# Optimization experiments

Measured on AMD Instinct MI355X. Metric: run time of the kernel, lower is better.

Reference implementation:

```python
import jax, jax.numpy as jnp
import numpy as np

B, S, H0G, H1G, H0E, H1E, A, E = 16384, 512, 512, 256, 1024, 512, 64, 4


def setup_inputs() -> dict:
    key = jax.random.key(0)
    ks = jax.random.split(key, 8)
    rn = lambda k, shape, s=0.05: jax.random.normal(k, shape, jnp.float32) * s
    return {
        "x": rn(ks[0], (B, S), 1.0),
        # Gating network params (Normalizer + 2 tanh layers + fca, softmax outside)
        "g_mean": jnp.zeros((S,), jnp.float32),
        "g_std": jnp.ones((S,), jnp.float32),
        "gW0": rn(ks[1], (S, H0G)), "gb0": jnp.zeros((H0G,), jnp.float32),
        "gW1": rn(ks[2], (H0G, H1G)), "gb1": jnp.zeros((H1G,), jnp.float32),
        "gWa": rn(ks[3], (H1G, E)), "gba": jnp.zeros((E,), jnp.float32),
        # 4 expert Actors, weights stacked along leading expert axis E
        "e_mean": jnp.zeros((E, S), jnp.float32),
        "e_std": jnp.ones((E, S), jnp.float32),
        "eW0": rn(ks[4], (E, S, H0E)), "eb0": jnp.zeros((E, H0E), jnp.float32),
        "eW1": rn(ks[5], (E, H0E, H1E)), "eb1": jnp.zeros((E, H1E), jnp.float32),
        "eWa": rn(ks[6], (E, H1E, A), 0.001), "eba": jnp.zeros((E, A), jnp.float32),
        "scale": jnp.ones((A,), jnp.float32),  # (a_max - a_min) / 2
    }


def reference(x, g_mean, g_std, gW0, gb0, gW1, gb1, gWa, gba,
              e_mean, e_std, eW0, eb0, eW1, eb1, eWa, eba, scale):
    # Gating: normalize -> tanh MLP -> linear -> softmax over experts
    xg = (x - g_mean) / g_std                                   # [B,S]
    h = jnp.tanh(xg @ gW0 + gb0)
    h = jnp.tanh(h @ gW1 + gb1)
    w = jax.nn.softmax(h @ gWa + gba, axis=-1)                  # [B,E]

    # Experts (Actor.forward), batched over expert axis e
    xe = (x[None, :, :] - e_mean[:, None, :]) / e_std[:, None, :]          # [E,B,S]
    he = jnp.tanh(jnp.einsum('ebs,esh->ebh', xe, eW0) + eb0[:, None, :])   # [E,B,H0E]
    he = jnp.tanh(jnp.einsum('ebh,ehk->ebk', he, eW1) + eb1[:, None, :])   # [E,B,H1E]
    a = (jnp.einsum('ebk,eka->eba', he, eWa) + eba[:, None, :]) * scale    # [E,B,A]

    # Weighted combination of expert action means
    return jnp.einsum('be,eba->ba', w, a)                       # [B,A]
```

## Files before the change

kernel.cpp:

```cpp
#include <hip/hip_runtime.h>
#include <hip/hip_bf16.h>

typedef _Float16 f16;
typedef _Float16 f16x4 __attribute__((ext_vector_type(4)));
typedef _Float16 f16x8 __attribute__((ext_vector_type(8)));
typedef float f32x4 __attribute__((ext_vector_type(4)));

#define DEV static __device__ __forceinline__

DEV void gld_lds16(const void* g, void* l) {
  __builtin_amdgcn_global_load_lds(
      (const __attribute__((address_space(1))) void*)g,
      (__attribute__((address_space(3))) void*)l, 16, 0, 0);
}

DEV float fast_tanh(float x) {
  float e = __expf(2.0f * x);
  return 1.0f - 2.0f / (e + 1.0f);
}

DEV int xcd_swizzle(int raw, int nwg) {
  return ((nwg & 7) == 0) ? ((raw & 7) * (nwg >> 3) + (raw >> 3)) : raw;
}

__global__ __launch_bounds__(256) void k_cvt_x(const float* __restrict__ x,
                                               f16* __restrict__ xh, long n) {
  long i0 = ((long)blockIdx.x * 256 + threadIdx.x) * 4;
  long stride = (long)gridDim.x * 1024;
  for (long i = i0; i < n; i += stride) {
    const float4 v = *(const float4*)(x + i);
    f16x4 h;
    h.x = (f16)v.x; h.y = (f16)v.y; h.z = (f16)v.z; h.w = (f16)v.w;
    *(f16x4*)(xh + i) = h;
  }
}

__global__ __launch_bounds__(256) void k_transpose(const float* __restrict__ in,
                                                   f16* __restrict__ out,
                                                   const float* __restrict__ stdv,
                                                   int K_, int N_) {
  __shared__ float tile[32][33];
  const int e = blockIdx.z;
  const float* ine = in + (long)e * K_ * N_;
  f16* oute = out + (long)e * K_ * N_;
  const int n0 = blockIdx.x * 32, k0 = blockIdx.y * 32;
  const int tx = threadIdx.x, ty = threadIdx.y;
#pragma unroll
  for (int j = 0; j < 4; j++)
    tile[ty + j * 8][tx] = ine[(long)(k0 + ty + j * 8) * N_ + n0 + tx];
  __syncthreads();
  const float rs = stdv ? 1.0f / stdv[(long)e * K_ + k0 + tx] : 1.0f;
#pragma unroll
  for (int j = 0; j < 4; j++)
    oute[(long)(n0 + ty + j * 8) * K_ + k0 + tx] = (f16)(tile[tx][ty + j * 8] * rs);
}

__global__ __launch_bounds__(1024) void k_bias_corr(const float* __restrict__ W,
                                                    const float* __restrict__ b,
                                                    const float* __restrict__ mean,
                                                    const float* __restrict__ stdv,
                                                    float* __restrict__ outb,
                                                    int S_, int H_) {
  __shared__ float red[16][64];
  const int e = blockIdx.y;
  const float* We = W + (long)e * S_ * H_;
  const float* me = mean + (long)e * S_;
  const float* se = stdv + (long)e * S_;
  const int h = blockIdx.x * 64 + threadIdx.x;
  const int sl = threadIdx.y;
  float acc = 0.0f;
#pragma unroll 4
  for (int s = sl; s < S_; s += 16) acc += (me[s] / se[s]) * We[(long)s * H_ + h];
  red[sl][threadIdx.x] = acc;
  __syncthreads();
  if (sl == 0) {
    float a = 0.0f;
#pragma unroll
    for (int j = 0; j < 16; j++) a += red[j][threadIdx.x];
    outb[(long)e * H_ + h] = b[(long)e * H_ + h] - a;
  }
}

__global__ __launch_bounds__(256) void k_gemm_cv(
    const f16* __restrict__ A, const f16* __restrict__ Bt,
    const float* __restrict__ bias, f16* __restrict__ C,
    int M, int K, int lda, int ldb, int ldc,
    long sA, long sB, long sBias, long sC) {
  A += (long)blockIdx.z * sA; Bt += (long)blockIdx.z * sB;
  bias += (long)blockIdx.z * sBias; C += (long)blockIdx.z * sC;
  extern __shared__ __align__(16) f16 lds[];
  const int tid = threadIdx.x, wave = tid >> 6, lane = tid & 63;
  const int nwg = gridDim.x * gridDim.y;
  const int logical = xcd_swizzle(blockIdx.y * gridDim.x + blockIdx.x, nwg);
  const int bx = logical % gridDim.x, by = logical / gridDim.x;
  const int m0 = by * 128, n0 = bx * 128;
  const int wr = wave >> 1, wc = wave & 1;
  f32x4 acc[4][4] = {};
  const int swz = (tid & 7) ^ ((tid >> 3) & 7);
  const f16* Ag = A + (long)(m0 + (tid >> 3)) * lda + swz * 8;
  const f16* Bg = Bt + (long)(n0 + (tid >> 3)) * ldb + swz * 8;
  const int wo = wave * 512;

#define STG_A(bufi, tile)                                         \
  { f16* _d = lds + (bufi) * 8192 + wo;                           \
    const long _k = (long)(tile) << 6;                            \
    gld_lds16(Ag + _k, _d);                                       \
    gld_lds16(Ag + (long)32 * lda + _k, _d + 2048);               \
    gld_lds16(Ag + (long)64 * lda + _k, _d + 4096);               \
    gld_lds16(Ag + (long)96 * lda + _k, _d + 6144); }
#define STG_B(bufi, tile)                                         \
  { f16* _d = lds + 24576 + (bufi) * 8192 + wo;                   \
    const long _k = (long)(tile) << 6;                            \
    gld_lds16(Bg + _k, _d);                                       \
    gld_lds16(Bg + (long)32 * ldb + _k, _d + 2048);               \
    gld_lds16(Bg + (long)64 * ldb + _k, _d + 4096);               \
    gld_lds16(Bg + (long)96 * ldb + _k, _d + 6144); }

  const int nt = K >> 6;
  STG_A(0, 0)
  STG_B(0, 0)
  STG_A(1, 1)
  asm volatile("s_waitcnt vmcnt(4)" ::: "memory");
  __builtin_amdgcn_s_barrier();
  asm volatile("" ::: "memory");

  for (int t = 0; t < nt; ++t) {
    if (t + 1 < nt) STG_B((t + 1) & 1, t + 1)
    if (t + 2 < nt) STG_A((t + 2) % 3, t + 2)
    const f16* Abuf = lds + (t % 3) * 8192;
    const f16* Bbuf = lds + 24576 + (t & 1) * 8192;
#pragma unroll
    for (int kk = 0; kk < 2; kk++) {
      f16x8 af[4], bfr[4];
      const int rchunk = (kk * 4 + (lane >> 4)) ^ (lane & 7);
#pragma unroll
      for (int mi = 0; mi < 4; mi++)
        af[mi] = *(const f16x8*)&Abuf[(wr * 64 + mi * 16 + (lane & 15)) * 64 + rchunk * 8];
#pragma unroll
      for (int ni = 0; ni < 4; ni++)
        bfr[ni] = *(const f16x8*)&Bbuf[(wc * 64 + ni * 16 + (lane & 15)) * 64 + rchunk * 8];
#pragma unroll
      for (int mi = 0; mi < 4; mi++)
#pragma unroll
        for (int ni = 0; ni < 4; ni++)
          acc[mi][ni] = __builtin_amdgcn_mfma_f32_16x16x32_f16(af[mi], bfr[ni], acc[mi][ni], 0, 0, 0);
    }
    if (t + 2 < nt) {
      asm volatile("s_waitcnt vmcnt(4)" ::: "memory");
    } else {
      asm volatile("s_waitcnt vmcnt(0)" ::: "memory");
    }
    __builtin_amdgcn_s_barrier();
    asm volatile("" ::: "memory");
  }
#undef STG_A
#undef STG_B

  const int r0 = (lane >> 4) * 4, cb = lane & 15;
#pragma unroll
  for (int ni = 0; ni < 4; ni++) {
    const int col = n0 + wc * 64 + ni * 16 + cb;
    const float bc = bias[col];
#pragma unroll
    for (int mi = 0; mi < 4; mi++) {
      const int row = m0 + wr * 64 + mi * 16 + r0;
#pragma unroll
      for (int r = 0; r < 4; r++)
        C[(long)(row + r) * ldc + col] = (f16)fast_tanh(acc[mi][ni][r] + bc);
    }
  }
}

__global__ __launch_bounds__(512, 2) void k_gemm_8p(
    const f16* __restrict__ A, const f16* __restrict__ Bt,
    const float* __restrict__ bias, f16* __restrict__ C,
    int M, int K, int lda, int ldb, int ldc,
    long sA, long sB, long sBias, long sC) {
  A += (long)blockIdx.z * sA; Bt += (long)blockIdx.z * sB;
  bias += (long)blockIdx.z * sBias; C += (long)blockIdx.z * sC;
  extern __shared__ __align__(16) f16 lds[];
  const int tid = threadIdx.x, wave = tid >> 6, lane = tid & 63;
  const int nwg = gridDim.x * gridDim.y;
  const int logical = xcd_swizzle(blockIdx.y * gridDim.x + blockIdx.x, nwg);
  const int bx = logical % gridDim.x, by = logical / gridDim.x;
  const int m0 = by * 256, n0 = bx * 256;
  const int wr = wave >> 2, wc = wave & 3;
  f32x4 acc[8][4] = {};

  const int swz = (tid & 7) ^ ((tid >> 3) & 7);
  const f16* Ag = A + (long)(m0 + (tid >> 3)) * lda + swz * 8;
  const f16* Bg = Bt + (long)(n0 + (tid >> 3)) * ldb + swz * 8;
  const int tdst = tid * 8;

  const int rc0 = (lane >> 4) ^ (lane & 7);
  const int rc1 = (4 + (lane >> 4)) ^ (lane & 7);
  int aoff[8], boff[4];
#pragma unroll
  for (int mi = 0; mi < 8; mi++) aoff[mi] = (wr * 128 + mi * 16 + (lane & 15)) * 64;
#pragma unroll
  for (int ni = 0; ni < 4; ni++) boff[ni] = 16384 + (wc * 64 + ni * 16 + (lane & 15)) * 64;

#define STG_A(jt, h)                                                          \
  { f16* _d = lds + ((jt) & 1) * 32768 + (h) * 8192 + tdst;                   \
    const long _k = (long)(jt) << 6;                                          \
    gld_lds16(Ag + (long)((h) * 128) * lda + _k, _d);                         \
    gld_lds16(Ag + (long)((h) * 128 + 64) * lda + _k, _d + 4096); }
#define STG_B(jt, h)                                                          \
  { f16* _d = lds + ((jt) & 1) * 32768 + 16384 + (h) * 8192 + tdst;           \
    const long _k = (long)(jt) << 6;                                          \
    gld_lds16(Bg + (long)((h) * 128) * ldb + _k, _d);                         \
    gld_lds16(Bg + (long)((h) * 128 + 64) * ldb + _k, _d + 4096); }
#define LOAD_A(b, rc)                                                         \
  _Pragma("unroll") for (int mi = 0; mi < 8; mi++)                            \
      af[mi] = *(const f16x8*)&lds[(b) * 32768 + aoff[mi] + (rc) * 8];
#define LOAD_B(b, ni, rc)                                                     \
  bfr[ni] = *(const f16x8*)&lds[(b) * 32768 + boff[ni] + (rc) * 8];
#define MMA2(nA, nB)                                                          \
  __builtin_amdgcn_s_setprio(1);                                              \
  _Pragma("unroll") for (int mi = 0; mi < 8; mi++) {                          \
    acc[mi][nA] = __builtin_amdgcn_mfma_f32_16x16x32_f16(af[mi], bfr[nA], acc[mi][nA], 0, 0, 0); \
    acc[mi][nB] = __builtin_amdgcn_mfma_f32_16x16x32_f16(af[mi], bfr[nB], acc[mi][nB], 0, 0, 0); \
  }                                                                           \
  __builtin_amdgcn_s_setprio(0);
#define BAR()                                                                 \
  __builtin_amdgcn_s_barrier();                                               \
  asm volatile("" ::: "memory")
#define WAITL()                                                               \
  asm volatile("s_waitcnt lgkmcnt(0)" ::: "memory");                          \
  __builtin_amdgcn_sched_barrier(0)

  const int nt = K >> 6;

  STG_A(0, 0) STG_A(0, 1) STG_B(0, 0) STG_B(0, 1)
  STG_A(1, 0)
  asm volatile("s_waitcnt vmcnt(2)" ::: "memory");
  BAR();

  f16x8 af[8], bfr[4];
  for (int j = 0; j < nt; ++j) {
    const int b = j & 1;
    LOAD_A(b, rc0) LOAD_B(b, 0, rc0) LOAD_B(b, 1, rc0)
    if (j + 1 < nt) STG_A(j + 1, 1)
    BAR(); WAITL(); MMA2(0, 1) BAR();
    LOAD_B(b, 2, rc0) LOAD_B(b, 3, rc0)
    if (j + 1 < nt) STG_B(j + 1, 0)
    BAR(); WAITL(); MMA2(2, 3) BAR();
    LOAD_A(b, rc1) LOAD_B(b, 0, rc1) LOAD_B(b, 1, rc1)
    if (j + 1 < nt) STG_B(j + 1, 1)
    BAR(); WAITL(); MMA2(0, 1) BAR();
    LOAD_B(b, 2, rc1) LOAD_B(b, 3, rc1)
    if (j + 2 < nt) STG_A(j + 2, 0)
    BAR(); WAITL(); MMA2(2, 3)
    if (j + 1 < nt) {
      if (j + 2 < nt) {
        asm volatile("s_waitcnt vmcnt(2)" ::: "memory");
      } else {
        asm volatile("s_waitcnt vmcnt(0)" ::: "memory");
      }
    }
    BAR();
  }
#undef STG_A
#undef STG_B
#undef LOAD_A
#undef LOAD_B
#undef MMA2
#undef BAR
#undef WAITL

  const int r0 = (lane >> 4) * 4, cb = lane & 15;
  float bcv[4];
#pragma unroll
  for (int ni = 0; ni < 4; ni++) bcv[ni] = bias[n0 + wc * 64 + ni * 16 + cb];
#pragma unroll
  for (int mi = 0; mi < 8; mi++) {
#pragma unroll
    for (int r = 0; r < 4; r++) {
      const long row = m0 + wr * 128 + mi * 16 + r0 + r;
#pragma unroll
      for (int ni = 0; ni < 4; ni++) {
        const int col = n0 + wc * 64 + ni * 16 + cb;
        C[row * (long)ldc + col] = (f16)fast_tanh(acc[mi][ni][r] + bcv[ni]);
      }
    }
  }
}

__global__ __launch_bounds__(256) void k_gating_head(const f16* __restrict__ h1,
                                                     const float* __restrict__ gWa,
                                                     const float* __restrict__ gba,
                                                     float* __restrict__ gw, int B_) {
  const int b = blockIdx.x * 4 + (threadIdx.x >> 6);
  const int lane = threadIdx.x & 63;
  const f16x4 hv = *(const f16x4*)&h1[(long)b * 256 + lane * 4];
  float s0 = 0, s1 = 0, s2 = 0, s3 = 0;
#pragma unroll
  for (int j = 0; j < 4; j++) {
    const float hh = (float)hv[j];
    const float4 wr4 = *(const float4*)&gWa[(lane * 4 + j) * 4];
    s0 += hh * wr4.x; s1 += hh * wr4.y; s2 += hh * wr4.z; s3 += hh * wr4.w;
  }
#pragma unroll
  for (int off = 32; off >= 1; off >>= 1) {
    s0 += __shfl_xor(s0, off);
    s1 += __shfl_xor(s1, off);
    s2 += __shfl_xor(s2, off);
    s3 += __shfl_xor(s3, off);
  }
  const float l0 = s0 + gba[0], l1 = s1 + gba[1], l2 = s2 + gba[2], l3 = s3 + gba[3];
  float mx = fmaxf(fmaxf(l0, l1), fmaxf(l2, l3));
  const float e0 = __expf(l0 - mx), e1 = __expf(l1 - mx), e2 = __expf(l2 - mx), e3 = __expf(l3 - mx);
  const float inv = 1.0f / (e0 + e1 + e2 + e3);
  if (lane == 0) {
    float4 o; o.x = e0 * inv; o.y = e1 * inv; o.z = e2 * inv; o.w = e3 * inv;
    *(float4*)&gw[(long)b * 4] = o;
  }
}

__global__ __launch_bounds__(256) void k_head2(const f16* __restrict__ he1,
                                               const f16* __restrict__ Wt,
                                               const float* __restrict__ eba,
                                               const float* __restrict__ scale,
                                               const float* __restrict__ gw,
                                               float* __restrict__ out,
                                               long sA) {
  constexpr int K = 512;
  __shared__ __align__(16) f16 As[2][64 * 64];
  __shared__ __align__(16) f16 Bs[2][64 * 64];
  const int tid = threadIdx.x, wave = tid >> 6, lane = tid & 63;
  const int bid = xcd_swizzle(blockIdx.x, gridDim.x);
  const long m0 = (long)bid * 64;
  const int swz = (tid & 7) ^ ((tid >> 3) & 7);
  const f16* Ag = he1 + (m0 + tid / 8) * K + swz * 8;
  const f16* Bg = Wt + (long)(tid / 8) * K + swz * 8;
  const int wo = wave * 512;
  const int r0 = (lane >> 4) * 4, cb = lane & 15;
  float4 gwv[4];
#pragma unroll
  for (int r = 0; r < 4; r++)
    gwv[r] = *(const float4*)&gw[(m0 + wave * 16 + r0 + r) * 4];
  f32x4 osum[4] = {};
  f32x4 acc[4] = {};

#pragma unroll
  for (int i = 0; i < 2; i++) {
    gld_lds16(Ag + (long)i * 32 * K, &As[0][wo + i * 2048]);
    gld_lds16(Bg + (long)i * 32 * K, &Bs[0][wo + i * 2048]);
  }
  __syncthreads();
  int cur = 0;
#pragma unroll
  for (int e = 0; e < 4; e++) {
    for (int kt = 0; kt < 8; ++kt) {
      const int s = e * 8 + kt;
      if (s + 1 < 32) {
        const int sn = s + 1;
        const long ae = (long)(sn >> 3) * sA + ((sn & 7) << 6);
        const long be = (long)(sn >> 3) * (64 * K) + ((sn & 7) << 6);
#pragma unroll
        for (int i = 0; i < 2; i++) {
          gld_lds16(Ag + ae + (long)i * 32 * K, &As[cur ^ 1][wo + i * 2048]);
          gld_lds16(Bg + be + (long)i * 32 * K, &Bs[cur ^ 1][wo + i * 2048]);
        }
      }
#pragma unroll
      for (int kk = 0; kk < 2; kk++) {
        const int rchunk = (kk * 4 + (lane >> 4)) ^ (lane & 7);
        const f16x8 a = *(const f16x8*)&As[cur][(wave * 16 + (lane & 15)) * 64 + rchunk * 8];
#pragma unroll
        for (int ni = 0; ni < 4; ni++) {
          const f16x8 bq = *(const f16x8*)&Bs[cur][(ni * 16 + (lane & 15)) * 64 + rchunk * 8];
          acc[ni] = __builtin_amdgcn_mfma_f32_16x16x32_f16(a, bq, acc[ni], 0, 0, 0);
        }
      }
      __syncthreads();
      cur ^= 1;
    }
#pragma unroll
    for (int ni = 0; ni < 4; ni++)
#pragma unroll
      for (int r = 0; r < 4; r++) {
        const float ge = (e == 0) ? gwv[r].x : (e == 1) ? gwv[r].y
                        : (e == 2) ? gwv[r].z : gwv[r].w;
        osum[ni][r] += ge * acc[ni][r];
        acc[ni][r] = 0.0f;
      }
  }

#pragma unroll
  for (int ni = 0; ni < 4; ni++) {
    const int col = ni * 16 + cb;
    const float sc = scale[col];
#pragma unroll
    for (int r = 0; r < 4; r++) {
      const long row = m0 + wave * 16 + r0 + r;
      const float b4 = gwv[r].x * eba[col] + gwv[r].y * eba[64 + col] +
                       gwv[r].z * eba[128 + col] + gwv[r].w * eba[192 + col];
      out[row * 64 + col] = (osum[ni][r] + b4) * sc;
    }
  }
}

__global__ __launch_bounds__(256) void k_head(const f16* __restrict__ he1,
                                              const f16* __restrict__ Wt,
                                              const float* __restrict__ ebae,
                                              const float* __restrict__ scale,
                                              const float* __restrict__ gw,
                                              float* __restrict__ outa,
                                              int e0, int K,
                                              long sA, long sB, long sBias, long sC) {
  const int z = blockIdx.z;
  he1 += (long)z * sA; Wt += (long)z * sB; ebae += (long)z * sBias; outa += (long)z * sC;
  const int e = e0 + z;
  __shared__ __align__(16) f16 As[2][64 * 64];
  __shared__ __align__(16) f16 Bs[2][64 * 64];
  const int tid = threadIdx.x, wave = tid >> 6, lane = tid & 63;
  const int bid = xcd_swizzle(blockIdx.x, gridDim.x);
  const long m0 = (long)bid * 64;
  f32x4 acc[4] = {};
  const int swz = (tid & 7) ^ ((tid >> 3) & 7);
  const f16* Ag = he1 + (m0 + tid / 8) * K + swz * 8;
  const f16* Bg = Wt + (long)(tid / 8) * K + swz * 8;
  const int wo = wave * 512;
#pragma unroll
  for (int i = 0; i < 2; i++) {
    gld_lds16(Ag + (long)i * 32 * K, &As[0][wo + i * 2048]);
    gld_lds16(Bg + (long)i * 32 * K, &Bs[0][wo + i * 2048]);
  }
  __syncthreads();
  const int nt = K >> 6;
  int cur = 0;
  for (int t = 0; t < nt; ++t) {
    if (t + 1 < nt) {
      const long kt = (long)(t + 1) << 6;
#pragma unroll
      for (int i = 0; i < 2; i++) {
        gld_lds16(Ag + (long)i * 32 * K + kt, &As[cur ^ 1][wo + i * 2048]);
        gld_lds16(Bg + (long)i * 32 * K + kt, &Bs[cur ^ 1][wo + i * 2048]);
      }
    }
#pragma unroll
    for (int kk = 0; kk < 2; kk++) {
      const int rchunk = (kk * 4 + (lane >> 4)) ^ (lane & 7);
      const f16x8 a = *(const f16x8*)&As[cur][(wave * 16 + (lane & 15)) * 64 + rchunk * 8];
#pragma unroll
      for (int ni = 0; ni < 4; ni++) {
        const f16x8 bq = *(const f16x8*)&Bs[cur][(ni * 16 + (lane & 15)) * 64 + rchunk * 8];
        acc[ni] = __builtin_amdgcn_mfma_f32_16x16x32_f16(a, bq, acc[ni], 0, 0, 0);
      }
    }
    __syncthreads();
    cur ^= 1;
  }
  const int r0 = (lane >> 4) * 4, cb = lane & 15;
#pragma unroll
  for (int ni = 0; ni < 4; ni++) {
    const int col = ni * 16 + cb;
    const float sb = scale[col], bb = ebae[col];
    const long row0 = m0 + wave * 16 + r0;
#pragma unroll
    for (int r = 0; r < 4; r++) {
      const long row = row0 + r;
      outa[row * 64 + col] = (acc[ni][r] + bb) * sb * gw[row * 4 + e];
    }
  }
}

__global__ __launch_bounds__(256) void k_combine(const float* __restrict__ a_all,
                                                 float* __restrict__ out, long n) {
  long i = ((long)blockIdx.x * 256 + threadIdx.x) * 4;
  if (i < n) {
    const float4 v0 = *(const float4*)(a_all + i);
    const float4 v1 = *(const float4*)(a_all + n + i);
    const float4 v2 = *(const float4*)(a_all + 2 * n + i);
    const float4 v3 = *(const float4*)(a_all + 3 * n + i);
    float4 o;
    o.x = v0.x + v1.x + v2.x + v3.x;
    o.y = v0.y + v1.y + v2.y + v3.y;
    o.z = v0.z + v1.z + v2.z + v3.z;
    o.w = v0.w + v1.w + v2.w + v3.w;
    *(float4*)(out + i) = o;
  }
}

extern "C" void kernel_launch(void* const* d_in, const int* in_sizes, int n_in,
                              void* d_out, int out_size, void* d_ws, size_t ws_size,
                              hipStream_t stream) {
  constexpr int Bn = 16384, S = 512, H0G = 512, H1G = 256, H0E = 1024, H1E = 512, A = 64, E = 4;
  const float* x      = (const float*)d_in[0];
  const float* g_mean = (const float*)d_in[1];
  const float* g_std  = (const float*)d_in[2];
  const float* gW0    = (const float*)d_in[3];
  const float* gb0    = (const float*)d_in[4];
  const float* gW1    = (const float*)d_in[5];
  const float* gb1    = (const float*)d_in[6];
  const float* gWa    = (const float*)d_in[7];
  const float* gba    = (const float*)d_in[8];
  const float* e_mean = (const float*)d_in[9];
  const float* e_std  = (const float*)d_in[10];
  const float* eW0    = (const float*)d_in[11];
  const float* eb0    = (const float*)d_in[12];
  const float* eW1    = (const float*)d_in[13];
  const float* eb1    = (const float*)d_in[14];
  const float* eWa    = (const float*)d_in[15];
  const float* eba    = (const float*)d_in[16];
  const float* scale  = (const float*)d_in[17];
  float* out = (float*)d_out;

  char* p = (char*)d_ws;
  auto alloc = [&](size_t bytes) { char* q = p; p += (bytes + 255) & ~(size_t)255; return q; };
  f16* xh    = (f16*)alloc((size_t)Bn * S * 2);
  float* gw  = (float*)alloc((size_t)Bn * E * 4);
  float* a_all = (float*)alloc((size_t)E * Bn * A * 4);
  f16* gW0t  = (f16*)alloc((size_t)S * H0G * 2);
  f16* gW1t  = (f16*)alloc((size_t)H0G * H1G * 2);
  f16* eW0t  = (f16*)alloc((size_t)E * S * H0E * 2);
  f16* eW1t  = (f16*)alloc((size_t)E * H0E * H1E * 2);
  f16* eWat  = (f16*)alloc((size_t)E * H1E * A * 2);
  float* gb0c = (float*)alloc((size_t)H0G * 4);
  float* eb0c = (float*)alloc((size_t)E * H0E * 4);
  f16* h0g   = (f16*)alloc((size_t)Bn * H0G * 2);
  const size_t base = (size_t)(p - (char*)d_ws);
  const size_t per_g = ((size_t)Bn * H0E * 2 + 256) + ((size_t)Bn * H1E * 2 + 256);
  int g = 1;
  if (ws_size >= base + 4 * per_g) g = 4;
  else if (ws_size >= base + 2 * per_g) g = 2;
  f16* he0_g = (f16*)alloc((size_t)g * Bn * H0E * 2);
  f16* he1_g = (f16*)alloc((size_t)g * Bn * H1E * 2);
  f16* h1g = he1_g;

  k_cvt_x<<<2048, 256, 0, stream>>>(x, xh, (long)Bn * S);
  k_transpose<<<dim3(H0G / 32, S / 32, 1), dim3(32, 8), 0, stream>>>(gW0, gW0t, g_std, S, H0G);
  k_transpose<<<dim3(H1G / 32, H0G / 32, 1), dim3(32, 8), 0, stream>>>(gW1, gW1t, nullptr, H0G, H1G);
  k_transpose<<<dim3(H0E / 32, S / 32, E), dim3(32, 8), 0, stream>>>(eW0, eW0t, e_std, S, H0E);
  k_transpose<<<dim3(H1E / 32, H0E / 32, E), dim3(32, 8), 0, stream>>>(eW1, eW1t, nullptr, H0E, H1E);
  k_transpose<<<dim3(A / 32, H1E / 32, E), dim3(32, 8), 0, stream>>>(eWa, eWat, nullptr, H1E, A);
  k_bias_corr<<<dim3(H0G / 64, 1), dim3(64, 16), 0, stream>>>(gW0, gb0, g_mean, g_std, gb0c, S, H0G);
  k_bias_corr<<<dim3(H0E / 64, E), dim3(64, 16), 0, stream>>>(eW0, eb0, e_mean, e_std, eb0c, S, H0E);

  constexpr size_t LDSCV = 5 * 128 * 64 * sizeof(f16);
  constexpr size_t LDS8P = 2 * 2 * 256 * 64 * sizeof(f16);

  k_gemm_cv<<<dim3(H0G / 128, Bn / 128, 1), 256, LDSCV, stream>>>(
      xh, gW0t, gb0c, h0g, Bn, S, S, S, H0G, 0, 0, 0, 0);
  k_gemm_cv<<<dim3(H1G / 128, Bn / 128, 1), 256, LDSCV, stream>>>(
      h0g, gW1t, gb1, h1g, Bn, H0G, H0G, H0G, H1G, 0, 0, 0, 0);
  k_gating_head<<<Bn / 4, 256, 0, stream>>>(h1g, gWa, gba, gw, Bn);

  if (g == 4) {
    k_gemm_8p<<<dim3(H0E / 256, Bn / 256, 4), 512, LDS8P, stream>>>(
        xh, eW0t, eb0c, he0_g, Bn, S, S, S, H0E,
        0, (long)S * H0E, H0E, (long)Bn * H0E);
    k_gemm_8p<<<dim3(H1E / 256, Bn / 256, 4), 512, LDS8P, stream>>>(
        he0_g, eW1t, eb1, he1_g, Bn, H0E, H0E, H0E, H1E,
        (long)Bn * H0E, (long)H0E * H1E, H1E, (long)Bn * H1E);
    k_head2<<<dim3(Bn / 64), 256, 0, stream>>>(
        he1_g, eWat, eba, scale, gw, out, (long)Bn * H1E);
  } else {
    for (int e0 = 0; e0 < E; e0 += g) {
      k_gemm_cv<<<dim3(H0E / 128, Bn / 128, g), 256, LDSCV, stream>>>(
          xh, eW0t + (size_t)e0 * S * H0E, eb0c + (size_t)e0 * H0E, he0_g,
          Bn, S, S, S, H0E,
          0, (long)S * H0E, H0E, (long)Bn * H0E);
      k_gemm_cv<<<dim3(H1E / 128, Bn / 128, g), 256, LDSCV, stream>>>(
          he0_g, eW1t + (size_t)e0 * H0E * H1E, eb1 + (size_t)e0 * H1E, he1_g,
          Bn, H0E, H0E, H0E, H1E,
          (long)Bn * H0E, (long)H0E * H1E, H1E, (long)Bn * H1E);
      k_head<<<dim3(Bn / 64, 1, g), 256, 0, stream>>>(
          he1_g, eWat + (size_t)e0 * H1E * A, eba + (size_t)e0 * A, scale, gw,
          a_all + (size_t)e0 * Bn * A, e0, H1E,
          (long)Bn * H1E, (long)H1E * A, A, (long)Bn * A);
    }
    k_combine<<<(Bn * A) / 1024, 256, 0, stream>>>(a_all, out, (long)Bn * A);
  }
}
```

Measured before the change: 293.9 us.

## Fold gating-network GEMMs and weight preprocessing into expert batched launches

The gating MLP's two GEMMs now ride as an extra z-slice of the expert k_gemm_8p launches, and the gating weight transposes and bias correction are merged into the expert launches via a zSplit dispatch. This removes separate small launches and lets the gating work fill idle CUs alongside the expert tiles, instead of running its own under-filled grids first. The added z-slice has fewer N tiles, so some blocks exit early, and h1g now gets its own buffer rather than aliasing he1_g.

After: 300.9 us. 1.02x slower.

```diff
diff --git a/kernel.cpp b/kernel.cpp
--- a/kernel.cpp
+++ b/kernel.cpp
@@ -33,6 +33,33 @@
     h.x = (f16)v.x; h.y = (f16)v.y; h.z = (f16)v.z; h.w = (f16)v.w;
     *(f16x4*)(xh + i) = h;
   }
+}
+
+__global__ __launch_bounds__(256) void k_transpose2(
+    const float* __restrict__ in, f16* __restrict__ out,
+    const float* __restrict__ stdv, int K_, int N_,
+    const float* __restrict__ in2, f16* __restrict__ out2,
+    const float* __restrict__ stdv2, int K2, int N2, int zSplit) {
+  __shared__ float tile[32][33];
+  const int z = blockIdx.z;
+  const float* inp; f16* outp; const float* sd; int KK, NN;
+  if (z >= zSplit) {
+    inp = in2; outp = out2; sd = stdv2; KK = K2; NN = N2;
+  } else {
+    inp = in + (long)z * K_ * N_; outp = out + (long)z * K_ * N_;
+    sd = stdv ? stdv + (long)z * K_ : nullptr; KK = K_; NN = N_;
+  }
+  const int n0 = blockIdx.x * 32, k0 = blockIdx.y * 32;
+  if (n0 >= NN || k0 >= KK) return;
+  const int tx = threadIdx.x, ty = threadIdx.y;
+#pragma unroll
+  for (int j = 0; j < 4; j++)
+    tile[ty + j * 8][tx] = inp[(long)(k0 + ty + j * 8) * NN + n0 + tx];
+  __syncthreads();
+  const float rs = sd ? 1.0f / sd[k0 + tx] : 1.0f;
+#pragma unroll
+  for (int j = 0; j < 4; j++)
+    outp[(long)(n0 + ty + j * 8) * KK + k0 + tx] = (f16)(tile[tx][ty + j * 8] * rs);
 }
 
 __global__ __launch_bounds__(256) void k_transpose(const float* __restrict__ in,
@@ -55,29 +82,37 @@
     oute[(long)(n0 + ty + j * 8) * K_ + k0 + tx] = (f16)(tile[tx][ty + j * 8] * rs);
 }
 
-__global__ __launch_bounds__(1024) void k_bias_corr(const float* __restrict__ W,
-                                                    const float* __restrict__ b,
-                                                    const float* __restrict__ mean,
-                                                    const float* __restrict__ stdv,
-                                                    float* __restrict__ outb,
-                                                    int S_, int H_) {
+__global__ __launch_bounds__(1024) void k_bias_corr2(
+    const float* __restrict__ W, const float* __restrict__ b,
+    const float* __restrict__ mean, const float* __restrict__ stdv,
+    float* __restrict__ outb, int S_, int H_,
+    const float* __restrict__ W2, const float* __restrict__ b2,
+    const float* __restrict__ mean2, const float* __restrict__ std2,
+    float* __restrict__ outb2, int H2, int zSplit) {
   __shared__ float red[16][64];
-  const int e = blockIdx.y;
-  const float* We = W + (long)e * S_ * H_;
-  const float* me = mean + (long)e * S_;
-  const float* se = stdv + (long)e * S_;
+  const int z = blockIdx.y;
+  const float* Wp; const float* bp; const float* mp; const float* sp;
+  float* op; int HH;
+  if (z >= zSplit) {
+    if ((int)(blockIdx.x * 64) >= H2) return;
+    Wp = W2; bp = b2; mp = mean2; sp = std2; op = outb2; HH = H2;
+  } else {
+    Wp = W + (long)z * S_ * H_; bp = b + (long)z * H_;
+    mp = mean + (long)z * S_; sp = stdv + (long)z * S_;
+    op = outb + (long)z * H_; HH = H_;
+  }
   const int h = blockIdx.x * 64 + threadIdx.x;
   const int sl = threadIdx.y;
   float acc = 0.0f;
 #pragma unroll 4
-  for (int s = sl; s < S_; s += 16) acc += (me[s] / se[s]) * We[(long)s * H_ + h];
+  for (int s = sl; s < S_; s += 16) acc += (mp[s] / sp[s]) * Wp[(long)s * HH + h];
   red[sl][threadIdx.x] = acc;
   __syncthreads();
   if (sl == 0) {
     float a = 0.0f;
 #pragma unroll
     for (int j = 0; j < 16; j++) a += red[j][threadIdx.x];
-    outb[(long)e * H_ + h] = b[(long)e * H_ + h] - a;
+    op[h] = bp[h] - a;
   }
 }
 
@@ -175,14 +210,23 @@
     const f16* __restrict__ A, const f16* __restrict__ Bt,
     const float* __restrict__ bias, f16* __restrict__ C,
     int M, int K, int lda, int ldb, int ldc,
-    long sA, long sB, long sBias, long sC) {
-  A += (long)blockIdx.z * sA; Bt += (long)blockIdx.z * sB;
-  bias += (long)blockIdx.z * sBias; C += (long)blockIdx.z * sC;
+    long sA, long sB, long sBias, long sC,
+    const f16* __restrict__ A2, const f16* __restrict__ B2,
+    const float* __restrict__ bias2, f16* __restrict__ C2,
+    int K2, int lda2, int ldb2, int ldc2, int nx2, int zSplit) {
   extern __shared__ __align__(16) f16 lds[];
   const int tid = threadIdx.x, wave = tid >> 6, lane = tid & 63;
   const int nwg = gridDim.x * gridDim.y;
   const int logical = xcd_swizzle(blockIdx.y * gridDim.x + blockIdx.x, nwg);
   const int bx = logical % gridDim.x, by = logical / gridDim.x;
+  if ((int)blockIdx.z >= zSplit) {
+    if (bx >= nx2) return;
+    A = A2; Bt = B2; bias = bias2; C = C2;
+    K = K2; lda = lda2; ldb = ldb2; ldc = ldc2;
+  } else {
+    A += (long)blockIdx.z * sA; Bt += (long)blockIdx.z * sB;
+    bias += (long)blockIdx.z * sBias; C += (long)blockIdx.z * sC;
+  }
   const int m0 = by * 256, n0 = bx * 256;
   const int wr = wave >> 2, wc = wave & 3;
   f32x4 acc[8][4] = {};
@@ -511,7 +555,6 @@
   auto alloc = [&](size_t bytes) { char* q = p; p += (bytes + 255) & ~(size_t)255; return q; };
   f16* xh    = (f16*)alloc((size_t)Bn * S * 2);
   float* gw  = (float*)alloc((size_t)Bn * E * 4);
-  float* a_all = (float*)alloc((size_t)E * Bn * A * 4);
   f16* gW0t  = (f16*)alloc((size_t)S * H0G * 2);
   f16* gW1t  = (f16*)alloc((size_t)H0G * H1G * 2);
   f16* eW0t  = (f16*)alloc((size_t)E * S * H0E * 2);
@@ -520,43 +563,47 @@
   float* gb0c = (float*)alloc((size_t)H0G * 4);
   float* eb0c = (float*)alloc((size_t)E * H0E * 4);
   f16* h0g   = (f16*)alloc((size_t)Bn * H0G * 2);
+  f16* h1g   = (f16*)alloc((size_t)Bn * H1G * 2);
   const size_t base = (size_t)(p - (char*)d_ws);
   const size_t per_g = ((size_t)Bn * H0E * 2 + 256) + ((size_t)Bn * H1E * 2 + 256);
+  const size_t aall_b = (size_t)E * Bn * A * 4 + 256;
   int g = 1;
   if (ws_size >= base + 4 * per_g) g = 4;
-  else if (ws_size >= base + 2 * per_g) g = 2;
+  else if (ws_size >= base + 2 * per_g + aall_b) g = 2;
   f16* he0_g = (f16*)alloc((size_t)g * Bn * H0E * 2);
   f16* he1_g = (f16*)alloc((size_t)g * Bn * H1E * 2);
-  f16* h1g = he1_g;
 
   k_cvt_x<<<2048, 256, 0, stream>>>(x, xh, (long)Bn * S);
-  k_transpose<<<dim3(H0G / 32, S / 32, 1), dim3(32, 8), 0, stream>>>(gW0, gW0t, g_std, S, H0G);
-  k_transpose<<<dim3(H1G / 32, H0G / 32, 1), dim3(32, 8), 0, stream>>>(gW1, gW1t, nullptr, H0G, H1G);
-  k_transpose<<<dim3(H0E / 32, S / 32, E), dim3(32, 8), 0, stream>>>(eW0, eW0t, e_std, S, H0E);
-  k_transpose<<<dim3(H1E / 32, H0E / 32, E), dim3(32, 8), 0, stream>>>(eW1, eW1t, nullptr, H0E, H1E);
+  k_transpose2<<<dim3(H0E / 32, S / 32, 5), dim3(32, 8), 0, stream>>>(
+      eW0, eW0t, e_std, S, H0E, gW0, gW0t, g_std, S, H0G, E);
+  k_transpose2<<<dim3(H1E / 32, H0E / 32, 5), dim3(32, 8), 0, stream>>>(
+      eW1, eW1t, nullptr, H0E, H1E, gW1, gW1t, nullptr, H0G, H1G, E);
   k_transpose<<<dim3(A / 32, H1E / 32, E), dim3(32, 8), 0, stream>>>(eWa, eWat, nullptr, H1E, A);
-  k_bias_corr<<<dim3(H0G / 64, 1), dim3(64, 16), 0, stream>>>(gW0, gb0, g_mean, g_std, gb0c, S, H0G);
-  k_bias_corr<<<dim3(H0E / 64, E), dim3(64, 16), 0, stream>>>(eW0, eb0, e_mean, e_std, eb0c, S, H0E);
+  k_bias_corr2<<<dim3(H0E / 64, 5), dim3(64, 16), 0, stream>>>(
+      eW0, eb0, e_mean, e_std, eb0c, S, H0E, gW0, gb0, g_mean, g_std, gb0c, H0G, E);
 
   constexpr size_t LDSCV = 5 * 128 * 64 * sizeof(f16);
   constexpr size_t LDS8P = 2 * 2 * 256 * 64 * sizeof(f16);
 
-  k_gemm_cv<<<dim3(H0G / 128, Bn / 128, 1), 256, LDSCV, stream>>>(
-      xh, gW0t, gb0c, h0g, Bn, S, S, S, H0G, 0, 0, 0, 0);
-  k_gemm_cv<<<dim3(H1G / 128, Bn / 128, 1), 256, LDSCV, stream>>>(
-      h0g, gW1t, gb1, h1g, Bn, H0G, H0G, H0G, H1G, 0, 0, 0, 0);
-  k_gating_head<<<Bn / 4, 256, 0, stream>>>(h1g, gWa, gba, gw, Bn);
-
   if (g == 4) {
-    k_gemm_8p<<<dim3(H0E / 256, Bn / 256, 4), 512, LDS8P, stream>>>(
+    k_gemm_8p<<<dim3(H0E / 256, Bn / 256, 5), 512, LDS8P, stream>>>(
         xh, eW0t, eb0c, he0_g, Bn, S, S, S, H0E,
-        0, (long)S * H0E, H0E, (long)Bn * H0E);
-    k_gemm_8p<<<dim3(H1E / 256, Bn / 256, 4), 512, LDS8P, stream>>>(
+        0, (long)S * H0E, H0E, (long)Bn * H0E,
+        xh, gW0t, gb0c, h0g, S, S, S, H0G, H0G / 256, E);
+    k_gemm_8p<<<dim3(H1E / 256, Bn / 256, 5), 512, LDS8P, stream>>>(
         he0_g, eW1t, eb1, he1_g, Bn, H0E, H0E, H0E, H1E,
-        (long)Bn * H0E, (long)H0E * H1E, H1E, (long)Bn * H1E);
+        (long)Bn * H0E, (long)H0E * H1E, H1E, (long)Bn * H1E,
+        h0g, gW1t, gb1, h1g, H0G, H0G, H0G, H1G, 1, E);
+    k_gating_head<<<Bn / 4, 256, 0, stream>>>(h1g, gWa, gba, gw, Bn);
     k_head2<<<dim3(Bn / 64), 256, 0, stream>>>(
         he1_g, eWat, eba, scale, gw, out, (long)Bn * H1E);
   } else {
+    float* a_all = (float*)alloc((size_t)E * Bn * A * 4);
+    k_gemm_cv<<<dim3(H0G / 128, Bn / 128, 1), 256, LDSCV, stream>>>(
+        xh, gW0t, gb0c, h0g, Bn, S, S, S, H0G, 0, 0, 0, 0);
+    k_gemm_cv<<<dim3(H1G / 128, Bn / 128, 1), 256, LDSCV, stream>>>(
+        h0g, gW1t, gb1, h1g, Bn, H0G, H0G, H0G, H1G, 0, 0, 0, 0);
+    k_gating_head<<<Bn / 4, 256, 0, stream>>>(h1g, gWa, gba, gw, Bn);
     for (int e0 = 0; e0 < E; e0 += g) {
       k_gemm_cv<<<dim3(H0E / 128, Bn / 128, g), 256, LDSCV, stream>>>(
           xh, eW0t + (size_t)e0 * S * H0E, eb0c + (size_t)e0 * H0E, he0_g,
```
